# Kernel optimization log

Measured on AMD Instinct MI355X. Metric: run time of the kernel, lower is better.

The kernel has to match this reference:

```python
import jax, jax.numpy as jnp
import numpy as np
from jax import lax

LENGTH = 9
PAD = LENGTH // 2          # 4
WIN_SIZE = LENGTH * LENGTH # 81
EPS = 1e-09
ALPHA = 0.01
PENALTY = 'l2'


def setup_inputs() -> dict:
    key = jax.random.key(0)
    k1, k2, k3 = jax.random.split(key, 3)
    B, C, H, W = 8, 1, 1024, 1024
    I = jax.random.normal(k1, (B, C, H, W), dtype=jnp.float32)
    J = jax.random.normal(k2, (B, C, H, W), dtype=jnp.float32)
    s = jax.random.normal(k3, (B, 2, H, W), dtype=jnp.float32)
    # buffer: all-ones box filter, shape [out=1, in=C, k, k]
    sum_filt = jnp.ones((1, C, LENGTH, LENGTH), dtype=jnp.float32)
    return {"I": I, "J": J, "s": s, "sum_filt": sum_filt}


def _box_conv(x, filt):
    # NCHW conv with 'same' padding (odd kernel), stride 1 -> [B,1,H,W]
    return lax.conv_general_dilated(
        x, filt, window_strides=(1, 1),
        padding=[(PAD, PAD), (PAD, PAD)],
        dimension_numbers=('NCHW', 'OIHW', 'NCHW'))


def _compute_local_sums(I, J, filt):
    I2, J2, IJ = I * I, J * J, I * J
    I_sum = _box_conv(I, filt)
    J_sum = _box_conv(J, filt)
    I2_sum = _box_conv(I2, filt)
    J2_sum = _box_conv(J2, filt)
    IJ_sum = _box_conv(IJ, filt)
    u_I = I_sum / WIN_SIZE
    u_J = J_sum / WIN_SIZE
    cross = IJ_sum - u_J * I_sum - u_I * J_sum + u_I * u_J * WIN_SIZE
    I_var = I2_sum - 2 * u_I * I_sum + u_I * u_I * WIN_SIZE
    J_var = J2_sum - 2 * u_J * J_sum + u_J * u_J * WIN_SIZE
    return I_var, J_var, cross


def _gradient_loss(s):
    dy = jnp.abs(s[:, :, 1:, :] - s[:, :, :-1, :])
    dx = jnp.abs(s[:, :, :, 1:] - s[:, :, :, :-1])
    if PENALTY == 'l2':
        dy = dy * dy
        dx = dx * dx
    return (jnp.mean(dx) + jnp.mean(dy)) / 2.0


def reference(I, J, s, sum_filt):
    I_var, J_var, cross = _compute_local_sums(I, J, sum_filt)
    cc = cross * cross / (I_var * J_var + EPS)
    ncc_loss = -jnp.mean(cc)
    smoothness_loss = _gradient_loss(s) * ALPHA
    total_loss = ncc_loss + smoothness_loss
    return (total_loss, ncc_loss, smoothness_loss)
```

## Files before the change

### kernel.cpp

```cpp
#include <hip/hip_runtime.h>

#define HH 1024
#define WW 1024
#define NB 8
#define TY 8
#define NSTRIPS (HH / TY)
#define NCC_BLOCKS (NB * NSTRIPS * 2)
#define SROWS 8
#define NROWS_S (NB * 2 * HH)
#define SM_BLOCKS ((NROWS_S / SROWS) * 2)


__device__ __forceinline__ void load_win(const float* __restrict__ row, int q, float w[12]) {
    const float4* r4 = (const float4*)row;
    float4 m = (q > 0) ? r4[q - 1] : float4{0.f, 0.f, 0.f, 0.f};
    float4 c = r4[q];
    float4 p = (q < WW / 4 - 1) ? r4[q + 1] : float4{0.f, 0.f, 0.f, 0.f};
    w[0] = m.x; w[1] = m.y; w[2] = m.z; w[3] = m.w;
    w[4] = c.x; w[5] = c.y; w[6] = c.z; w[7] = c.w;
    w[8] = p.x; w[9] = p.y; w[10] = p.z; w[11] = p.w;
}

template <bool ADD>
__device__ __forceinline__ void accum_regs(const float wI[12], const float wJ[12],
                                           float vsI[4], float vsJ[4],
                                           float vsI2[4], float vsJ2[4], float vsIJ[4]) {
    float sI = (((wI[0] + wI[1]) + (wI[2] + wI[3])) + ((wI[4] + wI[5]) + (wI[6] + wI[7]))) + wI[8];
    float sJ = (((wJ[0] + wJ[1]) + (wJ[2] + wJ[3])) + ((wJ[4] + wJ[5]) + (wJ[6] + wJ[7]))) + wJ[8];

    float s2Ia = wI[0] * wI[0], s2Ib = wI[1] * wI[1];
    float s2Ja = wJ[0] * wJ[0], s2Jb = wJ[1] * wJ[1];
    float sIJa = wI[0] * wJ[0], sIJb = wI[1] * wJ[1];
#pragma unroll
    for (int k = 2; k < 9; k += 2) {
        s2Ia = fmaf(wI[k], wI[k], s2Ia);
        s2Ja = fmaf(wJ[k], wJ[k], s2Ja);
        sIJa = fmaf(wI[k], wJ[k], sIJa);
        if (k + 1 < 9) {
            s2Ib = fmaf(wI[k + 1], wI[k + 1], s2Ib);
            s2Jb = fmaf(wJ[k + 1], wJ[k + 1], s2Jb);
            sIJb = fmaf(wI[k + 1], wJ[k + 1], sIJb);
        }
    }
    float s2I = s2Ia + s2Ib;
    float s2J = s2Ja + s2Jb;
    float sIJ = sIJa + sIJb;

#pragma unroll
    for (int c = 0; c < 4; ++c) {
        if (c > 0) {
            sI += wI[c + 8] - wI[c - 1];
            sJ += wJ[c + 8] - wJ[c - 1];
            s2I = fmaf(wI[c + 8], wI[c + 8], fmaf(-wI[c - 1], wI[c - 1], s2I));
            s2J = fmaf(wJ[c + 8], wJ[c + 8], fmaf(-wJ[c - 1], wJ[c - 1], s2J));
            sIJ = fmaf(wI[c + 8], wJ[c + 8], fmaf(-wI[c - 1], wJ[c - 1], sIJ));
        }
        if (ADD) { vsI[c] += sI; vsJ[c] += sJ; vsI2[c] += s2I; vsJ2[c] += s2J; vsIJ[c] += sIJ; }
        else     { vsI[c] -= sI; vsJ[c] -= sJ; vsI2[c] -= s2I; vsJ2[c] -= s2J; vsIJ[c] -= sIJ; }
    }
}

template <bool ADD>
__device__ __forceinline__ void accum_row(const float* __restrict__ Ib, const float* __restrict__ Jb,
                                          int y, int q,
                                          float vsI[4], float vsJ[4],
                                          float vsI2[4], float vsJ2[4], float vsIJ[4]) {
    if (y < 0 || y >= HH) return;
    float wI[12], wJ[12];
    load_win(Ib + (size_t)y * WW, q, wI);
    load_win(Jb + (size_t)y * WW, q, wJ);
    accum_regs<ADD>(wI, wJ, vsI, vsJ, vsI2, vsJ2, vsIJ);
}


__global__ __launch_bounds__(128) void fused_kernel(const float* __restrict__ I,
                                                    const float* __restrict__ J,
                                                    const float* __restrict__ S,
                                                    float* __restrict__ ws) {
    __shared__ float red[4];
    const int bid = blockIdx.x;
    const int t = threadIdx.x;
    const int lane = t & 63;
    const int wid = t >> 6;

    if (bid < NCC_BLOCKS) {
        const int b = bid >> 8;
        const int rem = bid & 255;
        const int strip = rem >> 1;
        const int half = rem & 1;
        const int y0 = strip * TY;
        const int q = (half << 7) + t;
        const float* Ib = I + (size_t)b * HH * WW;
        const float* Jb = J + (size_t)b * HH * WW;

        float vsI[4] = {0.f, 0.f, 0.f, 0.f};
        float vsJ[4] = {0.f, 0.f, 0.f, 0.f};
        float vsI2[4] = {0.f, 0.f, 0.f, 0.f};
        float vsJ2[4] = {0.f, 0.f, 0.f, 0.f};
        float vsIJ[4] = {0.f, 0.f, 0.f, 0.f};
        float ccacc = 0.f;

#pragma unroll 2
        for (int k = 0; k < 8; ++k)
            accum_row<true>(Ib, Jb, y0 - 4 + k, q, vsI, vsJ, vsI2, vsJ2, vsIJ);

        constexpr float RW = 1.0f / 81.0f;
#pragma unroll 2
        for (int k = 0; k < TY; ++k) {
            const int y = y0 + k;
            const int ya = y + 4;
            const int yr = y - 4;
            const bool va = (ya < HH);
            const bool vr = (yr >= 0);

            float wIa[12], wJa[12], wIr[12], wJr[12];
            if (va) { load_win(Ib + (size_t)ya * WW, q, wIa); load_win(Jb + (size_t)ya * WW, q, wJa); }
            if (vr) { load_win(Ib + (size_t)yr * WW, q, wIr); load_win(Jb + (size_t)yr * WW, q, wJr); }

            if (va) accum_regs<true>(wIa, wJa, vsI, vsJ, vsI2, vsJ2, vsIJ);

#pragma unroll
            for (int c = 0; c < 4; ++c) {
                const float Is = vsI[c], Js = vsJ[c];
                const float aI = Is * RW;
                const float aJ = Js * RW;
                const float cross = fmaf(-aI, Js, vsIJ[c]);
                const float Iv = fmaf(-aI, Is, vsI2[c]);
                const float Jv = fmaf(-aJ, Js, vsJ2[c]);
                const float den = fmaf(Iv, Jv, 1e-9f);
                float r = __builtin_amdgcn_rcpf(den);
                r = r * fmaf(-den, r, 2.0f);
                ccacc = fmaf(cross * cross, r, ccacc);
            }

            if (vr) accum_regs<false>(wIr, wJr, vsI, vsJ, vsI2, vsJ2, vsIJ);
        }

#pragma unroll
        for (int o = 32; o; o >>= 1) ccacc += __shfl_down(ccacc, o);
        if (lane == 0) red[wid] = ccacc;
        __syncthreads();
        if (t == 0) ws[bid] = red[0] + red[1];
    } else {
        const int sb = bid - NCC_BLOCKS;
        const int rowblk = sb >> 1;
        const int half = sb & 1;
        const int r0 = rowblk * SROWS;
        const int qq = (half << 7) + t;
        const float* base = S + (size_t)r0 * WW;
        float dxacc = 0.f, dyacc = 0.f;

        float4 v = ((const float4*)base)[qq];
#pragma unroll 2
        for (int k = 0; k < SROWS; ++k) {
            const int y = (r0 + k) & (HH - 1);
            const float* rp = base + (size_t)k * WW;
            float d0 = v.y - v.x, d1 = v.z - v.y, d2 = v.w - v.z;
            dxacc += d0 * d0 + d1 * d1 + d2 * d2;
            if (qq < 255) { const float vr = rp[4 * qq + 4]; const float d3 = vr - v.w; dxacc += d3 * d3; }
            if (y < HH - 1) {
                const float4 vn = ((const float4*)(rp + WW))[qq];
                const float e0 = vn.x - v.x, e1 = vn.y - v.y, e2 = vn.z - v.z, e3 = vn.w - v.w;
                dyacc += e0 * e0 + e1 * e1 + e2 * e2 + e3 * e3;
                v = vn;
            }
        }

#pragma unroll
        for (int o = 32; o; o >>= 1) {
            dxacc += __shfl_down(dxacc, o);
            dyacc += __shfl_down(dyacc, o);
        }
        if (lane == 0) { red[wid] = dxacc; red[2 + wid] = dyacc; }
        __syncthreads();
        if (t == 0) {
            ws[NCC_BLOCKS + sb] = red[0] + red[1];
            ws[NCC_BLOCKS + SM_BLOCKS + sb] = red[2] + red[3];
        }
    }
}


__global__ __launch_bounds__(256) void finalize_kernel(const float* __restrict__ ws,
                                                       float* __restrict__ out) {
    __shared__ double sd[256];
    __shared__ double res[3];
    const int t = threadIdx.x;
    double cc = 0.0, dx = 0.0, dy = 0.0;
    for (int i = t; i < NCC_BLOCKS; i += 256) cc += (double)ws[i];
    for (int i = t; i < SM_BLOCKS; i += 256) dx += (double)ws[NCC_BLOCKS + i];
    for (int i = t; i < SM_BLOCKS; i += 256) dy += (double)ws[NCC_BLOCKS + SM_BLOCKS + i];

    sd[t] = cc; __syncthreads();
    for (int s = 128; s; s >>= 1) { if (t < s) sd[t] += sd[t + s]; __syncthreads(); }
    if (t == 0) res[0] = sd[0];
    __syncthreads();
    sd[t] = dx; __syncthreads();
    for (int s = 128; s; s >>= 1) { if (t < s) sd[t] += sd[t + s]; __syncthreads(); }
    if (t == 0) res[1] = sd[0];
    __syncthreads();
    sd[t] = dy; __syncthreads();
    for (int s = 128; s; s >>= 1) { if (t < s) sd[t] += sd[t + s]; __syncthreads(); }
    if (t == 0) {
        res[2] = sd[0];
        const double ncc = -(res[0] / ((double)NB * 1.0 * HH * WW));
        const double mdx = res[1] / ((double)NB * 2.0 * HH * (WW - 1));
        const double mdy = res[2] / ((double)NB * 2.0 * (HH - 1) * WW);
        const double smooth = 0.01 * 0.5 * (mdx + mdy);
        out[0] = (float)(ncc + smooth);
        out[1] = (float)ncc;
        out[2] = (float)smooth;
    }
}

extern "C" void kernel_launch(void* const* d_in, const int* in_sizes, int n_in,
                              void* d_out, int out_size, void* d_ws, size_t ws_size,
                              hipStream_t stream) {
    const float* I = (const float*)d_in[0];
    const float* J = (const float*)d_in[1];
    const float* S = (const float*)d_in[2];
    float* ws = (float*)d_ws;
    float* out = (float*)d_out;

    fused_kernel<<<NCC_BLOCKS + SM_BLOCKS, 128, 0, stream>>>(I, J, S, ws);
    finalize_kernel<<<1, 256, 0, stream>>>(ws, out);
}
```

Before: 190.4 us.

## Use wave-sized blocks and share neighbor float4s via shuffles instead of loads

Switches the fused kernel to 64-thread single-wave blocks, each covering a quarter row, which removes the shared-memory reduction and __syncthreads. Neighbor float4 halos for the horizontal window now come from wave shuffles, with only edge lanes issuing an extra global load, which cuts redundant loads from three to about one per row. The smoothness part now processes 16 rows per block. The shuffles add cross-lane instructions, and the smaller blocks double the number of partial sums the finalize kernel must reduce.

New measurement: 202.9 us. 6.6% more time.

```diff
diff --git a/kernel.cpp b/kernel.cpp
--- a/kernel.cpp
+++ b/kernel.cpp
@@ -5,17 +5,27 @@
 #define NB 8
 #define TY 8
 #define NSTRIPS (HH / TY)
-#define NCC_BLOCKS (NB * NSTRIPS * 2)
-#define SROWS 8
+#define NCC_BLOCKS (NB * NSTRIPS * 4)
+#define SROWS 16
 #define NROWS_S (NB * 2 * HH)
-#define SM_BLOCKS ((NROWS_S / SROWS) * 2)
-
-
-__device__ __forceinline__ void load_win(const float* __restrict__ row, int q, float w[12]) {
+#define SM_BLOCKS ((NROWS_S / SROWS) * 4)
+
+
+__device__ __forceinline__ void load_win_shfl(const float* __restrict__ row, int q, int l,
+                                              float w[12]) {
     const float4* r4 = (const float4*)row;
-    float4 m = (q > 0) ? r4[q - 1] : float4{0.f, 0.f, 0.f, 0.f};
-    float4 c = r4[q];
-    float4 p = (q < WW / 4 - 1) ? r4[q + 1] : float4{0.f, 0.f, 0.f, 0.f};
+    const float4 c = r4[q];
+    float4 e = {0.f, 0.f, 0.f, 0.f};
+    const bool isL = (l == 0), isR = (l == 63);
+    if ((isL && q > 0) || (isR && q < WW / 4 - 1))
+        e = r4[isL ? q - 1 : q + 1];
+    float4 m, p;
+    m.x = __shfl_up(c.x, 1);  m.y = __shfl_up(c.y, 1);
+    m.z = __shfl_up(c.z, 1);  m.w = __shfl_up(c.w, 1);
+    p.x = __shfl_down(c.x, 1); p.y = __shfl_down(c.y, 1);
+    p.z = __shfl_down(c.z, 1); p.w = __shfl_down(c.w, 1);
+    if (isL) m = e;
+    if (isR) p = e;
     w[0] = m.x; w[1] = m.y; w[2] = m.z; w[3] = m.w;
     w[4] = c.x; w[5] = c.y; w[6] = c.z; w[7] = c.w;
     w[8] = p.x; w[9] = p.y; w[10] = p.z; w[11] = p.w;
@@ -62,34 +72,31 @@
 
 template <bool ADD>
 __device__ __forceinline__ void accum_row(const float* __restrict__ Ib, const float* __restrict__ Jb,
-                                          int y, int q,
+                                          int y, int q, int l,
                                           float vsI[4], float vsJ[4],
                                           float vsI2[4], float vsJ2[4], float vsIJ[4]) {
     if (y < 0 || y >= HH) return;
     float wI[12], wJ[12];
-    load_win(Ib + (size_t)y * WW, q, wI);
-    load_win(Jb + (size_t)y * WW, q, wJ);
+    load_win_shfl(Ib + (size_t)y * WW, q, l, wI);
+    load_win_shfl(Jb + (size_t)y * WW, q, l, wJ);
     accum_regs<ADD>(wI, wJ, vsI, vsJ, vsI2, vsJ2, vsIJ);
 }
 
 
-__global__ __launch_bounds__(128) void fused_kernel(const float* __restrict__ I,
-                                                    const float* __restrict__ J,
-                                                    const float* __restrict__ S,
-                                                    float* __restrict__ ws) {
-    __shared__ float red[4];
+__global__ __launch_bounds__(64) void fused_kernel(const float* __restrict__ I,
+                                                   const float* __restrict__ J,
+                                                   const float* __restrict__ S,
+                                                   float* __restrict__ ws) {
     const int bid = blockIdx.x;
-    const int t = threadIdx.x;
-    const int lane = t & 63;
-    const int wid = t >> 6;
+    const int l = threadIdx.x;
 
     if (bid < NCC_BLOCKS) {
-        const int b = bid >> 8;
-        const int rem = bid & 255;
-        const int strip = rem >> 1;
-        const int half = rem & 1;
+        const int b = bid >> 9;
+        const int rem = bid & 511;
+        const int strip = rem >> 2;
+        const int quarter = rem & 3;
         const int y0 = strip * TY;
-        const int q = (half << 7) + t;
+        const int q = (quarter << 6) + l;
         const float* Ib = I + (size_t)b * HH * WW;
         const float* Jb = J + (size_t)b * HH * WW;
 
@@ -102,7 +109,7 @@
 
 #pragma unroll 2
         for (int k = 0; k < 8; ++k)
-            accum_row<true>(Ib, Jb, y0 - 4 + k, q, vsI, vsJ, vsI2, vsJ2, vsIJ);
+            accum_row<true>(Ib, Jb, y0 - 4 + k, q, l, vsI, vsJ, vsI2, vsJ2, vsIJ);
 
         constexpr float RW = 1.0f / 81.0f;
 #pragma unroll 2
@@ -114,8 +121,10 @@
             const bool vr = (yr >= 0);
 
             float wIa[12], wJa[12], wIr[12], wJr[12];
-            if (va) { load_win(Ib + (size_t)ya * WW, q, wIa); load_win(Jb + (size_t)ya * WW, q, wJa); }
-            if (vr) { load_win(Ib + (size_t)yr * WW, q, wIr); load_win(Jb + (size_t)yr * WW, q, wJr); }
+            if (va) { load_win_shfl(Ib + (size_t)ya * WW, q, l, wIa);
+                      load_win_shfl(Jb + (size_t)ya * WW, q, l, wJa); }
+            if (vr) { load_win_shfl(Ib + (size_t)yr * WW, q, l, wIr);
+                      load_win_shfl(Jb + (size_t)yr * WW, q, l, wJr); }
 
             if (va) accum_regs<true>(wIa, wJa, vsI, vsJ, vsI2, vsJ2, vsIJ);
 
@@ -138,15 +147,13 @@
 
 #pragma unroll
         for (int o = 32; o; o >>= 1) ccacc += __shfl_down(ccacc, o);
-        if (lane == 0) red[wid] = ccacc;
-        __syncthreads();
-        if (t == 0) ws[bid] = red[0] + red[1];
+        if (l == 0) ws[bid] = ccacc;
     } else {
         const int sb = bid - NCC_BLOCKS;
-        const int rowblk = sb >> 1;
-        const int half = sb & 1;
+        const int rowblk = sb >> 2;
+        const int quarter = sb & 3;
         const int r0 = rowblk * SROWS;
-        const int qq = (half << 7) + t;
+        const int qq = (quarter << 6) + l;
         const float* base = S + (size_t)r0 * WW;
         float dxacc = 0.f, dyacc = 0.f;
 
@@ -171,11 +178,9 @@
             dxacc += __shfl_down(dxacc, o);
             dyacc += __shfl_down(dyacc, o);
         }
-        if (lane == 0) { red[wid] = dxacc; red[2 + wid] = dyacc; }
-        __syncthreads();
-        if (t == 0) {
-            ws[NCC_BLOCKS + sb] = red[0] + red[1];
-            ws[NCC_BLOCKS + SM_BLOCKS + sb] = red[2] + red[3];
+        if (l == 0) {
+            ws[NCC_BLOCKS + sb] = dxacc;
+            ws[NCC_BLOCKS + SM_BLOCKS + sb] = dyacc;
         }
     }
 }
@@ -222,6 +227,6 @@
     float* ws = (float*)d_ws;
     float* out = (float*)d_out;
 
-    fused_kernel<<<NCC_BLOCKS + SM_BLOCKS, 128, 0, stream>>>(I, J, S, ws);
+    fused_kernel<<<NCC_BLOCKS + SM_BLOCKS, 64, 0, stream>>>(I, J, S, ws);
     finalize_kernel<<<1, 256, 0, stream>>>(ws, out);
 }
```

## Prefetch incoming rows into LDS via async global_load_lds double buffering

Applied to the files above, without the earlier changes.

The incoming (y+4) rows of I and J are now staged per wave into double-buffered LDS with global_load_lds, one row ahead of use. Windows are read from LDS with halo entries, and manual vmcnt waits order the async loads. The aim is to overlap global latency with compute and to cut the three overlapping float4 global loads per row down to one plus a halo. It depends on hand-counted vmcnt values and sched barriers, which are fragile and could serialize or race if the count is wrong.

Measured after the change: 222.4 us. 16.8% more time.

```diff
diff --git a/kernel.cpp b/kernel.cpp
--- a/kernel.cpp
+++ b/kernel.cpp
@@ -10,6 +10,32 @@
 #define NROWS_S (NB * 2 * HH)
 #define SM_BLOCKS ((NROWS_S / SROWS) * 2)
 
+
+__device__ __forceinline__ void gload16(const float* g, float* l) {
+    __builtin_amdgcn_global_load_lds((const __attribute__((address_space(1))) void*)g,
+                                     (__attribute__((address_space(3))) void*)l, 16, 0, 0);
+}
+
+__device__ __forceinline__ void stage_row(const float* rowp, float* ldsimg, int q0w, int l) {
+    gload16(rowp + (size_t)(q0w + l) * 4, ldsimg);
+    if (l < 2) {
+        const int qh = (l == 0) ? (q0w > 0 ? q0w - 1 : 0)
+                                : (q0w + 64 < 256 ? q0w + 64 : 255);
+        gload16(rowp + (size_t)qh * 4, ldsimg + 256);
+    }
+}
+
+__device__ __forceinline__ void lds_win(const float* ldsimg, int l, int q, float w[12]) {
+    const float4* L4 = (const float4*)ldsimg;
+    float4 m = (l == 0) ? L4[64] : L4[l - 1];
+    float4 c = L4[l];
+    float4 p = (l == 63) ? L4[65] : L4[l + 1];
+    if (q == 0)   { m.x = m.y = m.z = m.w = 0.f; }
+    if (q == 255) { p.x = p.y = p.z = p.w = 0.f; }
+    w[0] = m.x; w[1] = m.y; w[2] = m.z; w[3] = m.w;
+    w[4] = c.x; w[5] = c.y; w[6] = c.z; w[7] = c.w;
+    w[8] = p.x; w[9] = p.y; w[10] = p.z; w[11] = p.w;
+}
 
 __device__ __forceinline__ void load_win(const float* __restrict__ row, int q, float w[12]) {
     const float4* r4 = (const float4*)row;
@@ -77,6 +103,7 @@
                                                     const float* __restrict__ J,
                                                     const float* __restrict__ S,
                                                     float* __restrict__ ws) {
+    __shared__ __align__(16) float lds[2][2][2][264];
     __shared__ float red[4];
     const int bid = blockIdx.x;
     const int t = threadIdx.x;
@@ -90,6 +117,7 @@
         const int half = rem & 1;
         const int y0 = strip * TY;
         const int q = (half << 7) + t;
+        const int q0w = (half << 7) + (wid << 6);
         const float* Ib = I + (size_t)b * HH * WW;
         const float* Jb = J + (size_t)b * HH * WW;
 
@@ -104,20 +132,48 @@
         for (int k = 0; k < 8; ++k)
             accum_row<true>(Ib, Jb, y0 - 4 + k, q, vsI, vsJ, vsI2, vsJ2, vsIJ);
 
+        asm volatile("s_waitcnt vmcnt(0)" ::: "memory");
+        __builtin_amdgcn_sched_barrier(0);
+        {
+            const float* Ir = Ib + (size_t)(y0 + 4) * WW;
+            const float* Jr = Jb + (size_t)(y0 + 4) * WW;
+            stage_row(Ir, &lds[wid][0][0][0], q0w, lane);
+            stage_row(Jr, &lds[wid][0][1][0], q0w, lane);
+        }
+
         constexpr float RW = 1.0f / 81.0f;
-#pragma unroll 2
-        for (int k = 0; k < TY; ++k) {
+
+        auto body = [&](int k, bool pre) {
             const int y = y0 + k;
-            const int ya = y + 4;
             const int yr = y - 4;
-            const bool va = (ya < HH);
             const bool vr = (yr >= 0);
-
-            float wIa[12], wJa[12], wIr[12], wJr[12];
-            if (va) { load_win(Ib + (size_t)ya * WW, q, wIa); load_win(Jb + (size_t)ya * WW, q, wJa); }
-            if (vr) { load_win(Ib + (size_t)yr * WW, q, wIr); load_win(Jb + (size_t)yr * WW, q, wJr); }
-
-            if (va) accum_regs<true>(wIa, wJa, vsI, vsJ, vsI2, vsJ2, vsIJ);
+            const int ysub = vr ? yr : 0;
+            float wIr[12], wJr[12];
+            load_win(Ib + (size_t)ysub * WW, q, wIr);
+            load_win(Jb + (size_t)ysub * WW, q, wJr);
+            __builtin_amdgcn_sched_barrier(0);
+
+            const int buf = k & 1;
+            if (pre) {
+                const int yn = y0 + k + 5;
+                const int ync = yn < HH ? yn : HH - 1;
+                const float* Ir = Ib + (size_t)ync * WW;
+                const float* Jr = Jb + (size_t)ync * WW;
+                stage_row(Ir, &lds[wid][buf ^ 1][0][0], q0w, lane);
+                stage_row(Jr, &lds[wid][buf ^ 1][1][0], q0w, lane);
+                asm volatile("s_waitcnt vmcnt(10)" ::: "memory");
+            } else {
+                asm volatile("s_waitcnt vmcnt(6)" ::: "memory");
+            }
+            __builtin_amdgcn_sched_barrier(0);
+
+            const bool va = (y + 4 < HH);
+            if (va) {
+                float wIa[12], wJa[12];
+                lds_win(&lds[wid][buf][0][0], lane, q, wIa);
+                lds_win(&lds[wid][buf][1][0], lane, q, wJa);
+                accum_regs<true>(wIa, wJa, vsI, vsJ, vsI2, vsJ2, vsIJ);
+            }
 
 #pragma unroll
             for (int c = 0; c < 4; ++c) {
@@ -134,7 +190,11 @@
             }
 
             if (vr) accum_regs<false>(wIr, wJr, vsI, vsJ, vsI2, vsJ2, vsIJ);
-        }
+        };
+
+#pragma unroll 2
+        for (int k = 0; k < TY - 1; ++k) body(k, true);
+        body(TY - 1, false);
 
 #pragma unroll
         for (int o = 32; o; o >>= 1) ccacc += __shfl_down(ccacc, o);
```
